# Optimization experiments

Measured on AMD Instinct MI355X. Metric: run time of the kernel, lower is better.

## Reference

```python
import jax, jax.numpy as jnp
import numpy as np

BATCH, FIELD_DIM, EMBED_DIM = 4096, 20000, 64


def setup_inputs() -> dict:
    key = jax.random.key(0)
    k_idx, k_w = jax.random.split(key)
    # multi-hot indicator matrix (values in {0,1})
    indices = jax.random.randint(k_idx, (BATCH, FIELD_DIM), 0, 2, dtype=jnp.int32)
    # kaiming_normal_ on (field_dim, embed_dim): std = sqrt(2 / fan_in), fan_in = embed_dim
    W = jax.random.normal(k_w, (FIELD_DIM, EMBED_DIM), dtype=jnp.float32) * np.sqrt(2.0 / EMBED_DIM)
    return {"indices": indices, "W": W}


def reference(indices, W):
    # Per row: gather embeddings at nonzero positions and sum ('sum' aggregate).
    # Equivalent to binary-mask @ W; rows with no nonzeros yield zeros naturally.
    mask = (indices != 0).astype(W.dtype)          # [B, F]
    out = jnp.einsum('bf,fd->bd', mask, W)         # [B, D]
    return out
```

## Files before the change

### kernel.cpp

```cpp
#include <hip/hip_runtime.h>
#include <hip/hip_bf16.h>

#define BATCH 4096
#define FIELD 20000
#define EMBED 64
#define KC     25
#define KSPAN  800
#define SPW    25
#define MTILES 256
#define LROW_STRIDE 26
#define WAVE_LDS (16 * LROW_STRIDE)

typedef __attribute__((ext_vector_type(4))) float  f32x4;
typedef __attribute__((ext_vector_type(8))) short  short8;
typedef __attribute__((ext_vector_type(4))) unsigned int u32x4;
typedef unsigned long long u64;

__device__ __forceinline__ unsigned bf16_rtne(float f) {
    unsigned u = __builtin_bit_cast(unsigned, f);
    return (u + 0x7FFFu + ((u >> 16) & 1u)) >> 16;
}

__global__ __launch_bounds__(256) void prep_w_kernel(const float* __restrict__ W,
                                                     unsigned int* __restrict__ Wswz,
                                                     float* __restrict__ out) {
    if (blockIdx.x < 512) {
        float2 z; z.x = 0.f; z.y = 0.f;
        ((float2*)out)[blockIdx.x * 256 + threadIdx.x] = z;
    }

    __shared__ float lds[32 * 65];
    const int t  = threadIdx.x;
    const int s0 = blockIdx.x;

    const float4* src = (const float4*)(W + (size_t)s0 * 2048);
    float4 a = src[t * 2 + 0];
    float4 b = src[t * 2 + 1];
    int l  = t * 8;
    int kl = l >> 6, c = l & 63;
    float* dst = lds + kl * 65 + c;
    dst[0] = a.x; dst[1] = a.y; dst[2] = a.z; dst[3] = a.w;
    dst[4] = b.x; dst[5] = b.y; dst[6] = b.z; dst[7] = b.w;
    __syncthreads();

    const int lane = t & 63, tq = t >> 6;
    const int khi = lane >> 4, lrow = lane & 15;
    const int col = tq * 16 + lrow;
    u32x4 o;
#pragma unroll
    for (int j2 = 0; j2 < 4; ++j2) {
        int kloc = khi * 8 + 2 * j2;
        float w0 = lds[kloc * 65 + col];
        float w1 = lds[(kloc + 1) * 65 + col];
        o[j2] = bf16_rtne(w0) | (bf16_rtne(w1) << 16);
    }
    *(u32x4*)(Wswz + ((size_t)(s0 * 4 + tq) * 64 + lane) * 4) = o;
}

__global__ __launch_bounds__(256) void emb_mfma_kernel(const int* __restrict__ idxm,
                                                       const unsigned int* __restrict__ Wswz,
                                                       float* __restrict__ out) {
    __shared__ unsigned lmask[4 * WAVE_LDS];
    const int lane  = threadIdx.x & 63;
    const int widx  = threadIdx.x >> 6;
    const int w     = blockIdx.x * 4 + widx;
    const int mtile = w % MTILES;
    const int kc    = w / MTILES;
    const int lrow  = lane & 15;
    const int khi   = lane >> 4;
    unsigned* lm = lmask + widx * WAVE_LDS;

    for (int r = 0; r < 16; ++r) {
        const int* rp = idxm + (size_t)(mtile * 16 + r) * FIELD + kc * KSPAN;
        int v[13];
#pragma unroll
        for (int c = 0; c < 12; ++c) v[c] = rp[c * 64 + lane];
        v[12] = 1;
        if (lane < 32) v[12] = rp[768 + lane];
#pragma unroll
        for (int c = 0; c < 12; ++c) {
            u64 b = __ballot(v[c] != 0);
            if (lane == 0)
                *(u64*)&lm[r * LROW_STRIDE + 2 * c] = b;
        }
        u64 bt = __ballot(v[12] != 0);
        if (lane == 0)
            lm[r * LROW_STRIDE + 24] = (unsigned)bt;
    }
    __syncthreads();

    const short8* pB = (const short8*)Wswz + (size_t)kc * SPW * 4 * 64 + lane;
    const unsigned* mrow = lm + lrow * LROW_STRIDE;

    f32x4 acc0 = {0.f, 0.f, 0.f, 0.f};
    f32x4 acc1 = acc0, acc2 = acc0, acc3 = acc0;

#pragma unroll 5
    for (int s = 0; s < SPW; ++s) {
        unsigned Mw = mrow[s];
        short8 b0 = pB[0], b1 = pB[64], b2 = pB[128], b3 = pB[192];
        pB += 256;

        unsigned mb = Mw >> (khi * 8);
        u32x4 av;
#pragma unroll
        for (int j = 0; j < 4; ++j)
            av[j] = (((mb >> (2 * j)) & 1u) ? 0x3F80u : 0u)
                  | (((mb >> (2 * j + 1)) & 1u) ? 0x3F800000u : 0u);
        short8 afrag = __builtin_bit_cast(short8, av);

        acc0 = __builtin_amdgcn_mfma_f32_16x16x32_bf16(afrag, b0, acc0, 0, 0, 0);
        acc1 = __builtin_amdgcn_mfma_f32_16x16x32_bf16(afrag, b1, acc1, 0, 0, 0);
        acc2 = __builtin_amdgcn_mfma_f32_16x16x32_bf16(afrag, b2, acc2, 0, 0, 0);
        acc3 = __builtin_amdgcn_mfma_f32_16x16x32_bf16(afrag, b3, acc3, 0, 0, 0);
    }

    float* obase = out + (size_t)mtile * 16 * EMBED;
#pragma unroll
    for (int i = 0; i < 4; ++i) {
        int orow = khi * 4 + i;
        atomicAdd(obase + (size_t)orow * EMBED +      lrow, acc0[i]);
        atomicAdd(obase + (size_t)orow * EMBED + 16 + lrow, acc1[i]);
        atomicAdd(obase + (size_t)orow * EMBED + 32 + lrow, acc2[i]);
        atomicAdd(obase + (size_t)orow * EMBED + 48 + lrow, acc3[i]);
    }
}

extern "C" void kernel_launch(void* const* d_in, const int* in_sizes, int n_in,
                              void* d_out, int out_size, void* d_ws, size_t ws_size,
                              hipStream_t stream) {
    const int*   idxm = (const int*)d_in[0];
    const float* W    = (const float*)d_in[1];
    float*       out  = (float*)d_out;
    unsigned int* Wswz = (unsigned int*)d_ws;

    hipLaunchKernelGGL(prep_w_kernel, dim3(FIELD / 32), dim3(256), 0, stream,
                       W, Wswz, out);
    hipLaunchKernelGGL(emb_mfma_kernel, dim3(MTILES * KC / 4), dim3(256), 0, stream,
                       idxm, Wswz, out);
}
```

Before: 90.11 us.

## Split mask bit-packing into a separate compress kernel feeding the MFMA kernel

Moves the int32-to-bitmask ballot compression out of the MFMA kernel into a dedicated kernel that writes packed 800-bit masks per row chunk to global workspace. The MFMA kernel then loads its row's mask words directly into registers, which drops the LDS staging, the barrier and the serial 16-row load loop, and fully unrolls the step loop. The compression kernel gets one wave per row chunk, so the 328 MB index read is spread across many more independent waves. The cost is an extra launch and a small global round trip for the packed masks.

```diff
diff --git a/kernel.cpp b/kernel.cpp
--- a/kernel.cpp
+++ b/kernel.cpp
@@ -8,8 +8,9 @@
 #define KSPAN  800
 #define SPW    25
 #define MTILES 256
-#define LROW_STRIDE 26
-#define WAVE_LDS (16 * LROW_STRIDE)
+#define MSTRIDE 28
+#define CHUNKS (BATCH * KC)
+#define WSWZ_BYTES (FIELD * EMBED * 2)
 
 typedef __attribute__((ext_vector_type(4))) float  f32x4;
 typedef __attribute__((ext_vector_type(8))) short  short8;
@@ -57,47 +58,73 @@
     *(u32x4*)(Wswz + ((size_t)(s0 * 4 + tq) * 64 + lane) * 4) = o;
 }
 
-__global__ __launch_bounds__(256) void emb_mfma_kernel(const int* __restrict__ idxm,
-                                                       const unsigned int* __restrict__ Wswz,
+__global__ __launch_bounds__(256) void compress_kernel(const int* __restrict__ idxm,
+                                                       unsigned* __restrict__ gm) {
+    const int lane = threadIdx.x & 63;
+    const int w    = blockIdx.x * 4 + (threadIdx.x >> 6);
+    const int row  = w / KC;
+    const int kc   = w % KC;
+    const int* rp  = idxm + (size_t)row * FIELD + kc * KSPAN;
+
+    int v[12];
+#pragma unroll
+    for (int c = 0; c < 12; ++c) v[c] = rp[c * 64 + lane];
+    int vt = 0;
+    if (lane < 32) vt = rp[768 + lane];
+
+    unsigned wd[25];
+#pragma unroll
+    for (int c = 0; c < 12; ++c) {
+        u64 b = __ballot(v[c] != 0);
+        wd[2 * c]     = (unsigned)b;
+        wd[2 * c + 1] = (unsigned)(b >> 32);
+    }
+    wd[24] = (unsigned)__ballot(vt != 0);
+
+    if (lane == 0) {
+        u32x4* dst = (u32x4*)(gm + (size_t)w * MSTRIDE);
+#pragma unroll
+        for (int i = 0; i < 6; ++i) {
+            u32x4 o = {wd[4 * i], wd[4 * i + 1], wd[4 * i + 2], wd[4 * i + 3]};
+            dst[i] = o;
+        }
+        u32x4 o6 = {wd[24], 0u, 0u, 0u};
+        dst[6] = o6;
+    }
+}
+
+__global__ __launch_bounds__(256) void emb_mfma_kernel(const unsigned* __restrict__ gm,
+                                                       const unsigned* __restrict__ Wswz,
                                                        float* __restrict__ out) {
-    __shared__ unsigned lmask[4 * WAVE_LDS];
     const int lane  = threadIdx.x & 63;
-    const int widx  = threadIdx.x >> 6;
-    const int w     = blockIdx.x * 4 + widx;
+    const int w     = blockIdx.x * 4 + (threadIdx.x >> 6);
     const int mtile = w % MTILES;
     const int kc    = w / MTILES;
     const int lrow  = lane & 15;
     const int khi   = lane >> 4;
-    unsigned* lm = lmask + widx * WAVE_LDS;
+    const int row   = mtile * 16 + lrow;
 
-    for (int r = 0; r < 16; ++r) {
-        const int* rp = idxm + (size_t)(mtile * 16 + r) * FIELD + kc * KSPAN;
-        int v[13];
-#pragma unroll
-        for (int c = 0; c < 12; ++c) v[c] = rp[c * 64 + lane];
-        v[12] = 1;
-        if (lane < 32) v[12] = rp[768 + lane];
-#pragma unroll
-        for (int c = 0; c < 12; ++c) {
-            u64 b = __ballot(v[c] != 0);
-            if (lane == 0)
-                *(u64*)&lm[r * LROW_STRIDE + 2 * c] = b;
-        }
-        u64 bt = __ballot(v[12] != 0);
-        if (lane == 0)
-            lm[r * LROW_STRIDE + 24] = (unsigned)bt;
+    const u32x4* mp = (const u32x4*)(gm + ((size_t)row * KC + kc) * MSTRIDE);
+    unsigned M[25];
+    {
+        u32x4 t0 = mp[0], t1 = mp[1], t2 = mp[2], t3 = mp[3], t4 = mp[4], t5 = mp[5], t6 = mp[6];
+        M[0]=t0.x;  M[1]=t0.y;  M[2]=t0.z;  M[3]=t0.w;
+        M[4]=t1.x;  M[5]=t1.y;  M[6]=t1.z;  M[7]=t1.w;
+        M[8]=t2.x;  M[9]=t2.y;  M[10]=t2.z; M[11]=t2.w;
+        M[12]=t3.x; M[13]=t3.y; M[14]=t3.z; M[15]=t3.w;
+        M[16]=t4.x; M[17]=t4.y; M[18]=t4.z; M[19]=t4.w;
+        M[20]=t5.x; M[21]=t5.y; M[22]=t5.z; M[23]=t5.w;
+        M[24]=t6.x;
     }
-    __syncthreads();
 
     const short8* pB = (const short8*)Wswz + (size_t)kc * SPW * 4 * 64 + lane;
-    const unsigned* mrow = lm + lrow * LROW_STRIDE;
 
     f32x4 acc0 = {0.f, 0.f, 0.f, 0.f};
     f32x4 acc1 = acc0, acc2 = acc0, acc3 = acc0;
 
-#pragma unroll 5
+#pragma unroll
     for (int s = 0; s < SPW; ++s) {
-        unsigned Mw = mrow[s];
+        unsigned Mw = M[s];
         short8 b0 = pB[0], b1 = pB[64], b2 = pB[128], b3 = pB[192];
         pB += 256;
 
@@ -132,10 +159,14 @@
     const int*   idxm = (const int*)d_in[0];
     const float* W    = (const float*)d_in[1];
     float*       out  = (float*)d_out;
+
     unsigned int* Wswz = (unsigned int*)d_ws;
+    unsigned*     gm   = (unsigned*)((char*)d_ws + WSWZ_BYTES);
 
     hipLaunchKernelGGL(prep_w_kernel, dim3(FIELD / 32), dim3(256), 0, stream,
                        W, Wswz, out);
+    hipLaunchKernelGGL(compress_kernel, dim3(CHUNKS / 4), dim3(256), 0, stream,
+                       idxm, gm);
     hipLaunchKernelGGL(emb_mfma_kernel, dim3(MTILES * KC / 4), dim3(256), 0, stream,
-                       idxm, Wswz, out);
+                       gm, Wswz, out);
 }
```

Result: slower. 102.3 us (+13.6%).
